# Performance work log

Measured on AMD Instinct MI355X. Metric: run time of the kernel, lower is better.

Reference implementation:

```python
import jax, jax.numpy as jnp
import numpy as np


def setup_inputs() -> dict:
    key = jax.random.key(0)
    k1, k2, k3 = jax.random.split(key, 3)
    B, H, S, D = 2, 8, 4096, 64
    queries = jax.random.normal(k1, (B, H, S, D), dtype=jnp.float32)
    keys = jax.random.normal(k2, (B, H, S, D), dtype=jnp.float32)
    values = jax.random.normal(k3, (B, H, S, D), dtype=jnp.float32)
    mask = jnp.zeros((1, 1, S, S), dtype=jnp.float32)
    return {"queries": queries, "keys": keys, "values": values, "d_k": D, "mask": mask}


def reference(queries, keys, values, d_k, mask):
    # scores: [B, H, Sq, Sk]
    scale = 1.0 / jnp.sqrt(jnp.asarray(d_k, dtype=queries.dtype))
    scores = jnp.einsum("bhqd,bhkd->bhqk", queries, keys) * scale
    scores = scores + (-1e9) * mask  # additive mask, broadcasts over B, H
    weights = jax.nn.softmax(scores, axis=-1)
    return jnp.einsum("bhqk,bhkd->bhqd", weights, values)
```

## Files before the change

kernel.cpp:

```cpp
#include <hip/hip_runtime.h>

#define S_LEN 4096
#define DHEAD 64
#define BK    64
#define NT    (S_LEN / BK)
#define NBH   16
#define KPAD  72
#define BQ    128
#define TILE_HALFS (BK * DHEAD)

typedef __fp16   pk16x2 __attribute__((ext_vector_type(2)));
typedef _Float16 half4v __attribute__((ext_vector_type(4)));
typedef _Float16 half8  __attribute__((ext_vector_type(8)));
typedef float    f32x4  __attribute__((ext_vector_type(4)));
typedef float    f32x16 __attribute__((ext_vector_type(16)));
typedef unsigned uint2v __attribute__((ext_vector_type(2)));

#define MFMA32(a, b, c) __builtin_amdgcn_mfma_f32_32x32x16_f16(a, b, c, 0, 0, 0)

__device__ __forceinline__ unsigned pk2u(float a, float b) {
    union { pk16x2 p; unsigned u; } x;
    x.p = __builtin_amdgcn_cvt_pkrtz(a, b);
    return x.u;
}

__device__ __forceinline__ uint2v pls(unsigned x, unsigned y) {
    return __builtin_amdgcn_permlane32_swap(x, y, false, false);
}
__device__ __forceinline__ float xmax32(float v) {
    uint2v r = pls(__float_as_uint(v), __float_as_uint(v));
    return fmaxf(__uint_as_float(r.x), __uint_as_float(r.y));
}
__device__ __forceinline__ float xadd32(float v) {
    uint2v r = pls(__float_as_uint(v), __float_as_uint(v));
    return __uint_as_float(r.x) + __uint_as_float(r.y);
}

__global__ void mask_flag_kernel(const float4* __restrict__ mask, int* __restrict__ flag) {
    const long stride = 2048L * 256;
    long i = (long)blockIdx.x * 256 + threadIdx.x;
    int nz = 0;
    #pragma unroll
    for (int it = 0; it < 8; ++it) {
        float4 a = mask[i + it * stride];
        nz |= (a.x != 0.f) | (a.y != 0.f) | (a.z != 0.f) | (a.w != 0.f);
    }
    if (__any(nz)) {
        if ((threadIdx.x & 63) == 0) atomicOr(flag, 1);
    }
}

__global__ __launch_bounds__(512, 2) void attn32f_kernel(
    const float* __restrict__ Q, const float* __restrict__ K,
    const float* __restrict__ V, const int* __restrict__ dkp,
    const float* __restrict__ mask, const int* __restrict__ maskflag,
    float* __restrict__ O)
{
    const int bid = blockIdx.x;
    const int L   = (bid & 7) * 64 + (bid >> 3);
    const int bh  = L >> 5;
    const int qt  = L & 31;

    const int tid  = threadIdx.x;
    const int hf   = tid >> 8;
    const int t    = tid & 255;
    const int w    = (tid >> 6) & 3;
    const int lane = tid & 63;
    const int l31  = lane & 31;
    const int h    = lane >> 5;
    const int cx   = lane & 7;
    const int vkey = (l31 ^ (l31 >> 3)) & 7;

    const int HT  = NT / 2;
    const int kt0 = hf * HT;

    const long gbase = (long)bh * S_LEN * DHEAD;
    const float* Qh = Q + gbase;
    const float* Kh = K + gbase;
    const float* Vh = V + gbase;

    const int q0 = qt * 128 + w * 32;
    const float csq  = rsqrtf((float)dkp[0]) * 1.44269504088896f;
    const float mfac = -1e9f * 1.44269504088896f;
    const bool use_mask = (maskflag[0] != 0);

    __shared__ __align__(16) _Float16 KT[2][2][TILE_HALFS];
    __shared__ __align__(16) _Float16 VT[2][2][TILE_HALFS];

    half8 qf[4];
    #pragma unroll
    for (int ks = 0; ks < 4; ++ks) {
        const float4* src = (const float4*)(Qh + (long)(q0 + l31) * DHEAD + ks * 16 + h * 8);
        float4 a = src[0], b = src[1];
        union { unsigned u[4]; half8 h8; } u;
        u.u[0] = pk2u(a.x * csq, a.y * csq);
        u.u[1] = pk2u(a.z * csq, a.w * csq);
        u.u[2] = pk2u(b.x * csq, b.y * csq);
        u.u[3] = pk2u(b.z * csq, b.w * csq);
        qf[ks] = u.h8;
    }

    const int kr  = t >> 2;
    const int ks4 = t & 3;
    const int vrp = t >> 3;
    const int vdq = t & 7;
    const float* Kb = Kh + (long)kr * DHEAD + ks4 * 16;
    const float* Vb = Vh + (long)(2 * vrp) * DHEAD + vdq * 8;
    const int kcol0 = (((2 * ks4)     ^ (kr & 7)) << 3);
    const int kcol1 = (((2 * ks4 + 1) ^ (kr & 7)) << 3);
    const int vd0   = vdq * 8;
    const int voct  = vrp >> 2;
    const int vlow  = (2 * vrp) & 7;

    float4 kf[4], vf[4];
    auto load_tile = [&](int kt) {
        const float4* kp  = (const float4*)(Kb + (long)kt * TILE_HALFS);
        kf[0] = kp[0]; kf[1] = kp[1]; kf[2] = kp[2]; kf[3] = kp[3];
        const float4* vp0 = (const float4*)(Vb + (long)kt * TILE_HALFS);
        const float4* vp1 = (const float4*)(Vb + (long)kt * TILE_HALFS + DHEAD);
        vf[0] = vp0[0]; vf[1] = vp0[1]; vf[2] = vp1[0]; vf[3] = vp1[1];
    };
    auto store_tile = [&](int bb) {
        union { unsigned u[4]; half8 h8; } u0, u1;
        u0.u[0] = pk2u(kf[0].x, kf[0].y);
        u0.u[1] = pk2u(kf[0].z, kf[0].w);
        u0.u[2] = pk2u(kf[1].x, kf[1].y);
        u0.u[3] = pk2u(kf[1].z, kf[1].w);
        u1.u[0] = pk2u(kf[2].x, kf[2].y);
        u1.u[1] = pk2u(kf[2].z, kf[2].w);
        u1.u[2] = pk2u(kf[3].x, kf[3].y);
        u1.u[3] = pk2u(kf[3].z, kf[3].w);
        *(half8*)&KT[hf][bb][kr * 64 + kcol0] = u0.h8;
        *(half8*)&KT[hf][bb][kr * 64 + kcol1] = u1.h8;
        _Float16* vt = &VT[hf][bb][0];
        #define VCOL(j) ((((voct ^ (j) ^ vdq) & 7) << 3) + vlow)
        *(pk16x2*)&vt[(vd0 + 0) * 64 + VCOL(0)] = __builtin_amdgcn_cvt_pkrtz(vf[0].x, vf[2].x);
        *(pk16x2*)&vt[(vd0 + 1) * 64 + VCOL(1)] = __builtin_amdgcn_cvt_pkrtz(vf[0].y, vf[2].y);
        *(pk16x2*)&vt[(vd0 + 2) * 64 + VCOL(2)] = __builtin_amdgcn_cvt_pkrtz(vf[0].z, vf[2].z);
        *(pk16x2*)&vt[(vd0 + 3) * 64 + VCOL(3)] = __builtin_amdgcn_cvt_pkrtz(vf[0].w, vf[2].w);
        *(pk16x2*)&vt[(vd0 + 4) * 64 + VCOL(4)] = __builtin_amdgcn_cvt_pkrtz(vf[1].x, vf[3].x);
        *(pk16x2*)&vt[(vd0 + 5) * 64 + VCOL(5)] = __builtin_amdgcn_cvt_pkrtz(vf[1].y, vf[3].y);
        *(pk16x2*)&vt[(vd0 + 6) * 64 + VCOL(6)] = __builtin_amdgcn_cvt_pkrtz(vf[1].z, vf[3].z);
        *(pk16x2*)&vt[(vd0 + 7) * 64 + VCOL(7)] = __builtin_amdgcn_cvt_pkrtz(vf[1].w, vf[3].w);
        #undef VCOL
    };

    f32x16 o0 = {0.f,0.f,0.f,0.f,0.f,0.f,0.f,0.f,0.f,0.f,0.f,0.f,0.f,0.f,0.f,0.f};
    f32x16 o1 = o0;
    float m_i = -INFINITY;
    float l_i = 0.0f;

    load_tile(kt0);
    store_tile(0);
    __syncthreads();

    for (int lt = 0; lt < HT; ++lt) {
        const int kt = kt0 + lt;
        const int b  = lt & 1;
        if (lt + 1 < HT) load_tile(kt + 1);

        f32x16 s0 = {0.f,0.f,0.f,0.f,0.f,0.f,0.f,0.f,0.f,0.f,0.f,0.f,0.f,0.f,0.f,0.f};
        f32x16 s1 = s0;
        __builtin_amdgcn_s_setprio(1);
        #pragma unroll
        for (int ks = 0; ks < 4; ++ks) {
            const int off = (((2 * ks + h) ^ cx) << 3);
            half8 a0 = *(const half8*)&KT[hf][b][(l31 << 6) + off];
            half8 a1 = *(const half8*)&KT[hf][b][2048 + (l31 << 6) + off];
            s0 = MFMA32(a0, qf[ks], s0);
            s1 = MFMA32(a1, qf[ks], s1);
        }
        __builtin_amdgcn_s_setprio(0);

        if (lt + 1 < HT) store_tile(b ^ 1);

        if (use_mask) {
            const float* mrow = mask + (long)(q0 + l31) * S_LEN + kt * BK;
            #pragma unroll
            for (int r = 0; r < 16; ++r) {
                const int k = (r & 3) + ((r >> 2) << 3) + (h << 2);
                s0[r] += mfac * mrow[k];
                s1[r] += mfac * mrow[32 + k];
            }
        }

        {
            float tt[8];
            #pragma unroll
            for (int i = 0; i < 8; ++i)
                tt[i] = fmaxf(fmaxf(s0[2*i], s0[2*i+1]), fmaxf(s1[2*i], s1[2*i+1]));
            float mx = fmaxf(fmaxf(fmaxf(tt[0], tt[1]), fmaxf(tt[2], tt[3])),
                             fmaxf(fmaxf(tt[4], tt[5]), fmaxf(tt[6], tt[7])));
            mx = xmax32(mx);
            const bool need = __any(mx > m_i + 8.0f);
            const float mnew = need ? fmaxf(m_i, mx) : m_i;
            float ra = 0.f, rb = 0.f;
            #pragma unroll
            for (int r = 0; r < 16; ++r) {
                float p0 = __builtin_amdgcn_exp2f(s0[r] - mnew);
                float p1 = __builtin_amdgcn_exp2f(s1[r] - mnew);
                s0[r] = p0; s1[r] = p1;
                ra += p0; rb += p1;
            }
            float rsum = xadd32(ra + rb);
            if (need) {
                const float alpha = __builtin_amdgcn_exp2f(m_i - mnew);
                #pragma unroll
                for (int r = 0; r < 16; ++r) {
                    const int qr = (r & 3) + ((r >> 2) << 3) + (h << 2);
                    float a_r = __shfl(alpha, qr, 64);
                    o0[r] *= a_r; o1[r] *= a_r;
                }
                l_i = alpha * l_i + rsum;
                m_i = mnew;
            } else {
                l_i += rsum;
            }
        }

        unsigned wp[16];
        #pragma unroll
        for (int d = 0; d < 8; ++d) {
            wp[d]     = pk2u(s0[2*d], s0[2*d+1]);
            wp[8 + d] = pk2u(s1[2*d], s1[2*d+1]);
        }

        __builtin_amdgcn_s_setprio(1);
        #pragma unroll
        for (int si = 0; si < 4; ++si) {
            const int bs = (si >> 1) * 8 + (si & 1) * 4;
            uint2v r0 = pls(wp[bs + 0], wp[bs + 2]);
            uint2v r1 = pls(wp[bs + 1], wp[bs + 3]);
            union { unsigned u[4]; half8 h8; } pa;
            pa.u[0] = r0.x; pa.u[1] = r1.x; pa.u[2] = r0.y; pa.u[3] = r1.y;
            const int voff = (((2 * si + h) ^ vkey) << 3);
            half8 v0 = *(const half8*)&VT[hf][b][(l31 << 6) + voff];
            half8 v1 = *(const half8*)&VT[hf][b][2048 + (l31 << 6) + (voff ^ 32)];
            o0 = MFMA32(pa.h8, v0, o0);
            o1 = MFMA32(pa.h8, v1, o1);
        }
        __builtin_amdgcn_s_setprio(0);

        if (lt + 1 < HT) __syncthreads();
    }

    float*  comb = (float*)&KT[0][0][0];
    float2* mlA  = (float2*)&VT[0][0][0];
    float2* mlB  = mlA + 128;

    __syncthreads();
    if (hf == 1) {
        #pragma unroll
        for (int r = 0; r < 16; ++r) {
            const int qr = (r & 3) + ((r >> 2) << 3) + (h << 2);
            comb[w * 2048 + qr * 64 + l31]      = o0[r];
            comb[w * 2048 + qr * 64 + 32 + l31] = o1[r];
        }
        if (h == 0) mlB[w * 32 + l31] = make_float2(m_i, l_i);
    } else {
        if (h == 0) mlA[w * 32 + l31] = make_float2(m_i, l_i);
    }
    __syncthreads();

    if (hf == 0) {
        float* dst = O + gbase;
        #pragma unroll
        for (int r = 0; r < 16; ++r) {
            const int qr = (r & 3) + ((r >> 2) << 3) + (h << 2);
            const float2 ml1 = mlA[w * 32 + qr];
            const float2 ml2 = mlB[w * 32 + qr];
            const float m   = fmaxf(ml1.x, ml2.x);
            const float a1  = __builtin_amdgcn_exp2f(ml1.x - m);
            const float a2  = __builtin_amdgcn_exp2f(ml2.x - m);
            const float inv = __builtin_amdgcn_rcpf(ml1.y * a1 + ml2.y * a2);
            const float p0  = comb[w * 2048 + qr * 64 + l31];
            const float p1  = comb[w * 2048 + qr * 64 + 32 + l31];
            const long row = (long)(q0 + qr) * DHEAD;
            dst[row + l31]      = (o0[r] * a1 + p0 * a2) * inv;
            dst[row + 32 + l31] = (o1[r] * a1 + p1 * a2) * inv;
        }
    }
}

__global__ __launch_bounds__(256, 2) void attn_kernel_fb(
    const float* __restrict__ Q, const float* __restrict__ K,
    const float* __restrict__ V, const int* __restrict__ dk,
    const float* __restrict__ mask, const int* __restrict__ maskflag,
    float* __restrict__ O)
{
    const int qt   = blockIdx.x;
    const int bh   = blockIdx.y;
    const int tid  = threadIdx.x;
    const int wave = tid >> 6;
    const int lane = tid & 63;
    const int l15  = lane & 15;
    const int quad = lane >> 4;

    const long base = (long)bh * S_LEN * DHEAD;
    const float* Qh = Q + base;
    const float* Kh = K + base;
    const float* Vh = V + base;
    float*       Oh = O + base;

    const int q0 = qt * BQ + wave * 32;
    const float csq  = rsqrtf((float)dk[0]) * 1.44269504088896f;
    const float mfac = -1e9f * 1.44269504088896f;
    const bool use_mask = (maskflag[0] != 0);

    __shared__ __align__(16) _Float16 Kt[2][BK][KPAD];
    __shared__ __align__(16) _Float16 Vt[2][DHEAD * KPAD];
    __shared__ __align__(16) _Float16 Pw[4][32][KPAD];

    half8 qf[2][2];
    #pragma unroll
    for (int f = 0; f < 2; ++f) {
        #pragma unroll
        for (int kc = 0; kc < 2; ++kc) {
            const float4* src = (const float4*)(Qh + (long)(q0 + f*16 + l15) * DHEAD + kc*32 + quad*8);
            float4 a = src[0], b = src[1];
            union { pk16x2 p[4]; half8 h; } u;
            u.p[0] = __builtin_amdgcn_cvt_pkrtz(a.x*csq, a.y*csq);
            u.p[1] = __builtin_amdgcn_cvt_pkrtz(a.z*csq, a.w*csq);
            u.p[2] = __builtin_amdgcn_cvt_pkrtz(b.x*csq, b.y*csq);
            u.p[3] = __builtin_amdgcn_cvt_pkrtz(b.z*csq, b.w*csq);
            qf[f][kc] = u.h;
        }
    }

    const int kr  = tid >> 2;
    const int ks  = tid & 3;
    const int vrp = tid >> 3;
    const int vdq = tid & 7;
    const float* Kb = Kh + (long)kr * DHEAD + ks * 16;
    const float* Vb = Vh + (long)(2 * vrp) * DHEAD + vdq * 8;
    const int vcol = (((vrp >> 2) ^ vdq) << 3) + ((2 * vrp) & 7);
    const int vd0  = vdq * 8;

    float4 kf[4], vf[4];
    auto load_tile = [&](int kt) {
        const float4* kp  = (const float4*)(Kb + (long)kt * BK * DHEAD);
        kf[0] = kp[0]; kf[1] = kp[1]; kf[2] = kp[2]; kf[3] = kp[3];
        const float4* vp0 = (const float4*)(Vb + (long)kt * BK * DHEAD);
        const float4* vp1 = (const float4*)(Vb + (long)kt * BK * DHEAD + DHEAD);
        vf[0] = vp0[0]; vf[1] = vp0[1]; vf[2] = vp1[0]; vf[3] = vp1[1];
    };
    auto store_tile = [&](int b) {
        union { pk16x2 p[4]; half8 h; } u0, u1;
        u0.p[0] = __builtin_amdgcn_cvt_pkrtz(kf[0].x, kf[0].y);
        u0.p[1] = __builtin_amdgcn_cvt_pkrtz(kf[0].z, kf[0].w);
        u0.p[2] = __builtin_amdgcn_cvt_pkrtz(kf[1].x, kf[1].y);
        u0.p[3] = __builtin_amdgcn_cvt_pkrtz(kf[1].z, kf[1].w);
        u1.p[0] = __builtin_amdgcn_cvt_pkrtz(kf[2].x, kf[2].y);
        u1.p[1] = __builtin_amdgcn_cvt_pkrtz(kf[2].z, kf[2].w);
        u1.p[2] = __builtin_amdgcn_cvt_pkrtz(kf[3].x, kf[3].y);
        u1.p[3] = __builtin_amdgcn_cvt_pkrtz(kf[3].z, kf[3].w);
        *(half8*)&Kt[b][kr][ks*16]     = u0.h;
        *(half8*)&Kt[b][kr][ks*16 + 8] = u1.h;
        _Float16* vt = &Vt[b][0];
        *(pk16x2*)&vt[(vd0+0)*KPAD + vcol] = __builtin_amdgcn_cvt_pkrtz(vf[0].x, vf[2].x);
        *(pk16x2*)&vt[(vd0+1)*KPAD + vcol] = __builtin_amdgcn_cvt_pkrtz(vf[0].y, vf[2].y);
        *(pk16x2*)&vt[(vd0+2)*KPAD + vcol] = __builtin_amdgcn_cvt_pkrtz(vf[0].z, vf[2].z);
        *(pk16x2*)&vt[(vd0+3)*KPAD + vcol] = __builtin_amdgcn_cvt_pkrtz(vf[0].w, vf[2].w);
        *(pk16x2*)&vt[(vd0+4)*KPAD + vcol] = __builtin_amdgcn_cvt_pkrtz(vf[1].x, vf[3].x);
        *(pk16x2*)&vt[(vd0+5)*KPAD + vcol] = __builtin_amdgcn_cvt_pkrtz(vf[1].y, vf[3].y);
        *(pk16x2*)&vt[(vd0+6)*KPAD + vcol] = __builtin_amdgcn_cvt_pkrtz(vf[1].z, vf[3].z);
        *(pk16x2*)&vt[(vd0+7)*KPAD + vcol] = __builtin_amdgcn_cvt_pkrtz(vf[1].w, vf[3].w);
    };

    f32x4 o[2][4];
    #pragma unroll
    for (int f = 0; f < 2; ++f)
        #pragma unroll
        for (int dt = 0; dt < 4; ++dt) o[f][dt] = (f32x4){0.f, 0.f, 0.f, 0.f};
    float m_i[2] = {-INFINITY, -INFINITY};
    float l_i[2] = {0.0f, 0.0f};

    load_tile(0);
    store_tile(0);
    __syncthreads();

    for (int kt = 0; kt < NT; ++kt) {
        const int b = kt & 1;
        if (kt + 1 < NT) load_tile(kt + 1);

        f32x4 st[2][4];
        #pragma unroll
        for (int f = 0; f < 2; ++f)
            #pragma unroll
            for (int nt = 0; nt < 4; ++nt) st[f][nt] = (f32x4){0.f,0.f,0.f,0.f};
        #pragma unroll
        for (int nt = 0; nt < 4; ++nt) {
            #pragma unroll
            for (int kc = 0; kc < 2; ++kc) {
                half8 af = *(const half8*)&Kt[b][nt*16 + l15][kc*32 + quad*8];
                st[0][nt] = __builtin_amdgcn_mfma_f32_16x16x32_f16(af, qf[0][kc], st[0][nt], 0, 0, 0);
                st[1][nt] = __builtin_amdgcn_mfma_f32_16x16x32_f16(af, qf[1][kc], st[1][nt], 0, 0, 0);
            }
        }

        if (use_mask) {
            #pragma unroll
            for (int f = 0; f < 2; ++f) {
                const long mrow = (long)(q0 + f*16 + l15) * S_LEN + kt*BK;
                #pragma unroll
                for (int nt = 0; nt < 4; ++nt)
                    #pragma unroll
                    for (int r = 0; r < 4; ++r)
                        st[f][nt][r] += mfac * mask[mrow + nt*16 + quad*4 + r];
            }
        }

        float alpha[2];
        #pragma unroll
        for (int f = 0; f < 2; ++f) {
            float mx = fmaxf(fmaxf(fmaxf(st[f][0][0], st[f][0][1]), fmaxf(st[f][0][2], st[f][0][3])),
                             fmaxf(fmaxf(st[f][1][0], st[f][1][1]), fmaxf(st[f][1][2], st[f][1][3])));
            float mx2 = fmaxf(fmaxf(fmaxf(st[f][2][0], st[f][2][1]), fmaxf(st[f][2][2], st[f][2][3])),
                              fmaxf(fmaxf(st[f][3][0], st[f][3][1]), fmaxf(st[f][3][2], st[f][3][3])));
            mx = fmaxf(mx, mx2);
            mx = fmaxf(mx, __shfl_xor(mx, 16, 64));
            mx = fmaxf(mx, __shfl_xor(mx, 32, 64));
            float mnew = fmaxf(m_i[f], mx);
            float rsum = 0.0f;
            #pragma unroll
            for (int nt = 0; nt < 4; ++nt) {
                #pragma unroll
                for (int r = 0; r < 4; ++r) {
                    float p = __builtin_amdgcn_exp2f(st[f][nt][r] - mnew);
                    st[f][nt][r] = p;
                    rsum += p;
                }
            }
            rsum += __shfl_xor(rsum, 16, 64);
            rsum += __shfl_xor(rsum, 32, 64);
            alpha[f] = __builtin_amdgcn_exp2f(m_i[f] - mnew);
            l_i[f] = alpha[f] * l_i[f] + rsum;
            m_i[f] = mnew;
        }

        #pragma unroll
        for (int f = 0; f < 2; ++f)
            #pragma unroll
            for (int r = 0; r < 4; ++r) {
                float a_r = __shfl(alpha[f], quad*4 + r, 64);
                #pragma unroll
                for (int dt = 0; dt < 4; ++dt) o[f][dt][r] *= a_r;
            }

        #pragma unroll
        for (int f = 0; f < 2; ++f)
            #pragma unroll
            for (int nt = 0; nt < 4; ++nt) {
                union { pk16x2 p[2]; half4v h; } up;
                up.p[0] = __builtin_amdgcn_cvt_pkrtz(st[f][nt][0], st[f][nt][1]);
                up.p[1] = __builtin_amdgcn_cvt_pkrtz(st[f][nt][2], st[f][nt][3]);
                *(half4v*)&Pw[wave][f*16 + l15][nt*16 + quad*4] = up.h;
            }

        #pragma unroll
        for (int kc2 = 0; kc2 < 2; ++kc2) {
            half8 pa0 = *(const half8*)&Pw[wave][l15][kc2*32 + quad*8];
            half8 pa1 = *(const half8*)&Pw[wave][16 + l15][kc2*32 + quad*8];
            #pragma unroll
            for (int dt = 0; dt < 4; ++dt) {
                const int row = dt*16 + l15;
                const int pb  = (4*kc2 + quad) ^ (row >> 3);
                half8 vb = *(const half8*)&Vt[b][row*KPAD + pb*8];
                o[0][dt] = __builtin_amdgcn_mfma_f32_16x16x32_f16(pa0, vb, o[0][dt], 0, 0, 0);
                o[1][dt] = __builtin_amdgcn_mfma_f32_16x16x32_f16(pa1, vb, o[1][dt], 0, 0, 0);
            }
        }

        if (kt + 1 < NT) {
            store_tile((kt + 1) & 1);
            __syncthreads();
        }
    }

    #pragma unroll
    for (int f = 0; f < 2; ++f) {
        #pragma unroll
        for (int r = 0; r < 4; ++r) {
            float lq = __shfl(l_i[f], quad*4 + r, 64);
            float linv = __builtin_amdgcn_rcpf(lq);
            const long row = (long)(q0 + f*16 + quad*4 + r) * DHEAD;
            #pragma unroll
            for (int dt = 0; dt < 4; ++dt)
                Oh[row + dt*16 + l15] = o[f][dt][r] * linv;
        }
    }
}

extern "C" void kernel_launch(void* const* d_in, const int* in_sizes, int n_in,
                              void* d_out, int out_size, void* d_ws, size_t ws_size,
                              hipStream_t stream) {
    const float* Q    = (const float*)d_in[0];
    const float* K    = (const float*)d_in[1];
    const float* V    = (const float*)d_in[2];
    const int*   dk   = (const int*)d_in[3];
    const float* mask = (const float*)d_in[4];
    float* out = (float*)d_out;
    int* flag = (int*)d_ws;

    (void)hipMemsetAsync(flag, 0, sizeof(int), stream);
    mask_flag_kernel<<<2048, 256, 0, stream>>>((const float4*)mask, flag);

    if (ws_size >= 256) {
        attn32f_kernel<<<512, 512, 0, stream>>>(Q, K, V, dk, mask, flag, out);
    } else {
        dim3 grid(S_LEN / BQ, NBH);
        attn_kernel_fb<<<grid, 256, 0, stream>>>(Q, K, V, dk, mask, flag, out);
    }
}
```

Measured before the change: 281.3 us.

## Drop split-K two-half workgroups; run single 256-thread block over all key tiles

```diff
diff --git a/kernel.cpp b/kernel.cpp
--- a/kernel.cpp
+++ b/kernel.cpp
@@ -4,15 +4,10 @@
 #define DHEAD 64
 #define BK    64
 #define NT    (S_LEN / BK)
-#define NBH   16
-#define KPAD  72
-#define BQ    128
 #define TILE_HALFS (BK * DHEAD)
 
 typedef __fp16   pk16x2 __attribute__((ext_vector_type(2)));
-typedef _Float16 half4v __attribute__((ext_vector_type(4)));
 typedef _Float16 half8  __attribute__((ext_vector_type(8)));
-typedef float    f32x4  __attribute__((ext_vector_type(4)));
 typedef float    f32x16 __attribute__((ext_vector_type(16)));
 typedef unsigned uint2v __attribute__((ext_vector_type(2)));
 
@@ -50,7 +45,7 @@
     }
 }
 
-__global__ __launch_bounds__(512, 2) void attn32f_kernel(
+__global__ __launch_bounds__(256, 2) void attn32s_kernel(
     const float* __restrict__ Q, const float* __restrict__ K,
     const float* __restrict__ V, const int* __restrict__ dkp,
     const float* __restrict__ mask, const int* __restrict__ maskflag,
@@ -62,18 +57,13 @@
     const int qt  = L & 31;
 
     const int tid  = threadIdx.x;
-    const int hf   = tid >> 8;
-    const int t    = tid & 255;
-    const int w    = (tid >> 6) & 3;
+    const int w    = tid >> 6;
     const int lane = tid & 63;
     const int l31  = lane & 31;
     const int h    = lane >> 5;
     const int cx   = lane & 7;
     const int vkey = (l31 ^ (l31 >> 3)) & 7;
 
-    const int HT  = NT / 2;
-    const int kt0 = hf * HT;
-
     const long gbase = (long)bh * S_LEN * DHEAD;
     const float* Qh = Q + gbase;
     const float* Kh = K + gbase;
@@ -84,8 +74,8 @@
     const float mfac = -1e9f * 1.44269504088896f;
     const bool use_mask = (maskflag[0] != 0);
 
-    __shared__ __align__(16) _Float16 KT[2][2][TILE_HALFS];
-    __shared__ __align__(16) _Float16 VT[2][2][TILE_HALFS];
+    __shared__ __align__(16) _Float16 KT[2][TILE_HALFS];
+    __shared__ __align__(16) _Float16 VT[2][TILE_HALFS];
 
     half8 qf[4];
     #pragma unroll
@@ -100,10 +90,10 @@
         qf[ks] = u.h8;
     }
 
-    const int kr  = t >> 2;
-    const int ks4 = t & 3;
-    const int vrp = t >> 3;
-    const int vdq = t & 7;
+    const int kr  = tid >> 2;
+    const int ks4 = tid & 3;
+    const int vrp = tid >> 3;
+    const int vdq = tid & 7;
     const float* Kb = Kh + (long)kr * DHEAD + ks4 * 16;
     const float* Vb = Vh + (long)(2 * vrp) * DHEAD + vdq * 8;
     const int kcol0 = (((2 * ks4)     ^ (kr & 7)) << 3);
@@ -130,9 +120,9 @@
         u1.u[1] = pk2u(kf[2].z, kf[2].w);
         u1.u[2] = pk2u(kf[3].x, kf[3].y);
         u1.u[3] = pk2u(kf[3].z, kf[3].w);
-        *(half8*)&KT[hf][bb][kr * 64 + kcol0] = u0.h8;
-        *(half8*)&KT[hf][bb][kr * 64 + kcol1] = u1.h8;
-        _Float16* vt = &VT[hf][bb][0];
+        *(half8*)&KT[bb][kr * 64 + kcol0] = u0.h8;
+        *(half8*)&KT[bb][kr * 64 + kcol1] = u1.h8;
+        _Float16* vt = &VT[bb][0];
         #define VCOL(j) ((((voct ^ (j) ^ vdq) & 7) << 3) + vlow)
         *(pk16x2*)&vt[(vd0 + 0) * 64 + VCOL(0)] = __builtin_amdgcn_cvt_pkrtz(vf[0].x, vf[2].x);
         *(pk16x2*)&vt[(vd0 + 1) * 64 + VCOL(1)] = __builtin_amdgcn_cvt_pkrtz(vf[0].y, vf[2].y);
@@ -150,14 +140,13 @@
     float m_i = -INFINITY;
     float l_i = 0.0f;
 
-    load_tile(kt0);
+    load_tile(0);
     store_tile(0);
     __syncthreads();
 
-    for (int lt = 0; lt < HT; ++lt) {
-        const int kt = kt0 + lt;
-        const int b  = lt & 1;
-        if (lt + 1 < HT) load_tile(kt + 1);
+    for (int kt = 0; kt < NT; ++kt) {
+        const int b = kt & 1;
+        if (kt + 1 < NT) load_tile(kt + 1);
 
         f32x16 s0 = {0.f,0.f,0.f,0.f,0.f,0.f,0.f,0.f,0.f,0.f,0.f,0.f,0.f,0.f,0.f,0.f};
         f32x16 s1 = s0;
@@ -165,14 +154,14 @@
         #pragma unroll
         for (int ks = 0; ks < 4; ++ks) {
             const int off = (((2 * ks + h) ^ cx) << 3);
-            half8 a0 = *(const half8*)&KT[hf][b][(l31 << 6) + off];
-            half8 a1 = *(const half8*)&KT[hf][b][2048 + (l31 << 6) + off];
+            half8 a0 = *(const half8*)&KT[b][(l31 << 6) + off];
+            half8 a1 = *(const half8*)&KT[b][2048 + (l31 << 6) + off];
             s0 = MFMA32(a0, qf[ks], s0);
             s1 = MFMA32(a1, qf[ks], s1);
         }
         __builtin_amdgcn_s_setprio(0);
 
-        if (lt + 1 < HT) store_tile(b ^ 1);
+        if (kt + 1 < NT) store_tile(b ^ 1);
 
         if (use_mask) {
             const float* mrow = mask + (long)(q0 + l31) * S_LEN + kt * BK;
@@ -234,260 +223,25 @@
             union { unsigned u[4]; half8 h8; } pa;
             pa.u[0] = r0.x; pa.u[1] = r1.x; pa.u[2] = r0.y; pa.u[3] = r1.y;
             const int voff = (((2 * si + h) ^ vkey) << 3);
-            half8 v0 = *(const half8*)&VT[hf][b][(l31 << 6) + voff];
-            half8 v1 = *(const half8*)&VT[hf][b][2048 + (l31 << 6) + (voff ^ 32)];
+            half8 v0 = *(const half8*)&VT[b][(l31 << 6) + voff];
+            half8 v1 = *(const half8*)&VT[b][2048 + (l31 << 6) + (voff ^ 32)];
             o0 = MFMA32(pa.h8, v0, o0);
             o1 = MFMA32(pa.h8, v1, o1);
         }
         __builtin_amdgcn_s_setprio(0);
 
-        if (lt + 1 < HT) __syncthreads();
-    }
-
-    float*  comb = (float*)&KT[0][0][0];
-    float2* mlA  = (float2*)&VT[0][0][0];
-    float2* mlB  = mlA + 128;
-
-    __syncthreads();
-    if (hf == 1) {
-        #pragma unroll
-        for (int r = 0; r < 16; ++r) {
-            const int qr = (r & 3) + ((r >> 2) << 3) + (h << 2);
-            comb[w * 2048 + qr * 64 + l31]      = o0[r];
-            comb[w * 2048 + qr * 64 + 32 + l31] = o1[r];
-        }
-        if (h == 0) mlB[w * 32 + l31] = make_float2(m_i, l_i);
-    } else {
-        if (h == 0) mlA[w * 32 + l31] = make_float2(m_i, l_i);
-    }
-    __syncthreads();
-
-    if (hf == 0) {
-        float* dst = O + gbase;
-        #pragma unroll
-        for (int r = 0; r < 16; ++r) {
-            const int qr = (r & 3) + ((r >> 2) << 3) + (h << 2);
-            const float2 ml1 = mlA[w * 32 + qr];
-            const float2 ml2 = mlB[w * 32 + qr];
-            const float m   = fmaxf(ml1.x, ml2.x);
-            const float a1  = __builtin_amdgcn_exp2f(ml1.x - m);
-            const float a2  = __builtin_amdgcn_exp2f(ml2.x - m);
-            const float inv = __builtin_amdgcn_rcpf(ml1.y * a1 + ml2.y * a2);
-            const float p0  = comb[w * 2048 + qr * 64 + l31];
-            const float p1  = comb[w * 2048 + qr * 64 + 32 + l31];
-            const long row = (long)(q0 + qr) * DHEAD;
-            dst[row + l31]      = (o0[r] * a1 + p0 * a2) * inv;
-            dst[row + 32 + l31] = (o1[r] * a1 + p1 * a2) * inv;
-        }
-    }
-}
-
-__global__ __launch_bounds__(256, 2) void attn_kernel_fb(
-    const float* __restrict__ Q, const float* __restrict__ K,
-    const float* __restrict__ V, const int* __restrict__ dk,
-    const float* __restrict__ mask, const int* __restrict__ maskflag,
-    float* __restrict__ O)
-{
-    const int qt   = blockIdx.x;
-    const int bh   = blockIdx.y;
-    const int tid  = threadIdx.x;
-    const int wave = tid >> 6;
-    const int lane = tid & 63;
-    const int l15  = lane & 15;
-    const int quad = lane >> 4;
-
-    const long base = (long)bh * S_LEN * DHEAD;
-    const float* Qh = Q + base;
-    const float* Kh = K + base;
-    const float* Vh = V + base;
-    float*       Oh = O + base;
-
-    const int q0 = qt * BQ + wave * 32;
-    const float csq  = rsqrtf((float)dk[0]) * 1.44269504088896f;
-    const float mfac = -1e9f * 1.44269504088896f;
-    const bool use_mask = (maskflag[0] != 0);
-
-    __shared__ __align__(16) _Float16 Kt[2][BK][KPAD];
-    __shared__ __align__(16) _Float16 Vt[2][DHEAD * KPAD];
-    __shared__ __align__(16) _Float16 Pw[4][32][KPAD];
-
-    half8 qf[2][2];
+        if (kt + 1 < NT) __syncthreads();
+    }
+
+    float* dst = O + gbase;
     #pragma unroll
-    for (int f = 0; f < 2; ++f) {
-        #pragma unroll
-        for (int kc = 0; kc < 2; ++kc) {
-            const float4* src = (const float4*)(Qh + (long)(q0 + f*16 + l15) * DHEAD + kc*32 + quad*8);
-            float4 a = src[0], b = src[1];
-            union { pk16x2 p[4]; half8 h; } u;
-            u.p[0] = __builtin_amdgcn_cvt_pkrtz(a.x*csq, a.y*csq);
-            u.p[1] = __builtin_amdgcn_cvt_pkrtz(a.z*csq, a.w*csq);
-            u.p[2] = __builtin_amdgcn_cvt_pkrtz(b.x*csq, b.y*csq);
-            u.p[3] = __builtin_amdgcn_cvt_pkrtz(b.z*csq, b.w*csq);
-            qf[f][kc] = u.h;
-        }
-    }
-
-    const int kr  = tid >> 2;
-    const int ks  = tid & 3;
-    const int vrp = tid >> 3;
-    const int vdq = tid & 7;
-    const float* Kb = Kh + (long)kr * DHEAD + ks * 16;
-    const float* Vb = Vh + (long)(2 * vrp) * DHEAD + vdq * 8;
-    const int vcol = (((vrp >> 2) ^ vdq) << 3) + ((2 * vrp) & 7);
-    const int vd0  = vdq * 8;
-
-    float4 kf[4], vf[4];
-    auto load_tile = [&](int kt) {
-        const float4* kp  = (const float4*)(Kb + (long)kt * BK * DHEAD);
-        kf[0] = kp[0]; kf[1] = kp[1]; kf[2] = kp[2]; kf[3] = kp[3];
-        const float4* vp0 = (const float4*)(Vb + (long)kt * BK * DHEAD);
-        const float4* vp1 = (const float4*)(Vb + (long)kt * BK * DHEAD + DHEAD);
-        vf[0] = vp0[0]; vf[1] = vp0[1]; vf[2] = vp1[0]; vf[3] = vp1[1];
-    };
-    auto store_tile = [&](int b) {
-        union { pk16x2 p[4]; half8 h; } u0, u1;
-        u0.p[0] = __builtin_amdgcn_cvt_pkrtz(kf[0].x, kf[0].y);
-        u0.p[1] = __builtin_amdgcn_cvt_pkrtz(kf[0].z, kf[0].w);
-        u0.p[2] = __builtin_amdgcn_cvt_pkrtz(kf[1].x, kf[1].y);
-        u0.p[3] = __builtin_amdgcn_cvt_pkrtz(kf[1].z, kf[1].w);
-        u1.p[0] = __builtin_amdgcn_cvt_pkrtz(kf[2].x, kf[2].y);
-        u1.p[1] = __builtin_amdgcn_cvt_pkrtz(kf[2].z, kf[2].w);
-        u1.p[2] = __builtin_amdgcn_cvt_pkrtz(kf[3].x, kf[3].y);
-        u1.p[3] = __builtin_amdgcn_cvt_pkrtz(kf[3].z, kf[3].w);
-        *(half8*)&Kt[b][kr][ks*16]     = u0.h;
-        *(half8*)&Kt[b][kr][ks*16 + 8] = u1.h;
-        _Float16* vt = &Vt[b][0];
-        *(pk16x2*)&vt[(vd0+0)*KPAD + vcol] = __builtin_amdgcn_cvt_pkrtz(vf[0].x, vf[2].x);
-        *(pk16x2*)&vt[(vd0+1)*KPAD + vcol] = __builtin_amdgcn_cvt_pkrtz(vf[0].y, vf[2].y);
-        *(pk16x2*)&vt[(vd0+2)*KPAD + vcol] = __builtin_amdgcn_cvt_pkrtz(vf[0].z, vf[2].z);
-        *(pk16x2*)&vt[(vd0+3)*KPAD + vcol] = __builtin_amdgcn_cvt_pkrtz(vf[0].w, vf[2].w);
-        *(pk16x2*)&vt[(vd0+4)*KPAD + vcol] = __builtin_amdgcn_cvt_pkrtz(vf[1].x, vf[3].x);
-        *(pk16x2*)&vt[(vd0+5)*KPAD + vcol] = __builtin_amdgcn_cvt_pkrtz(vf[1].y, vf[3].y);
-        *(pk16x2*)&vt[(vd0+6)*KPAD + vcol] = __builtin_amdgcn_cvt_pkrtz(vf[1].z, vf[3].z);
-        *(pk16x2*)&vt[(vd0+7)*KPAD + vcol] = __builtin_amdgcn_cvt_pkrtz(vf[1].w, vf[3].w);
-    };
-
-    f32x4 o[2][4];
-    #pragma unroll
-    for (int f = 0; f < 2; ++f)
-        #pragma unroll
-        for (int dt = 0; dt < 4; ++dt) o[f][dt] = (f32x4){0.f, 0.f, 0.f, 0.f};
-    float m_i[2] = {-INFINITY, -INFINITY};
-    float l_i[2] = {0.0f, 0.0f};
-
-    load_tile(0);
-    store_tile(0);
-    __syncthreads();
-
-    for (int kt = 0; kt < NT; ++kt) {
-        const int b = kt & 1;
-        if (kt + 1 < NT) load_tile(kt + 1);
-
-        f32x4 st[2][4];
-        #pragma unroll
-        for (int f = 0; f < 2; ++f)
-            #pragma unroll
-            for (int nt = 0; nt < 4; ++nt) st[f][nt] = (f32x4){0.f,0.f,0.f,0.f};
-        #pragma unroll
-        for (int nt = 0; nt < 4; ++nt) {
-            #pragma unroll
-            for (int kc = 0; kc < 2; ++kc) {
-                half8 af = *(const half8*)&Kt[b][nt*16 + l15][kc*32 + quad*8];
-                st[0][nt] = __builtin_amdgcn_mfma_f32_16x16x32_f16(af, qf[0][kc], st[0][nt], 0, 0, 0);
-                st[1][nt] = __builtin_amdgcn_mfma_f32_16x16x32_f16(af, qf[1][kc], st[1][nt], 0, 0, 0);
-            }
-        }
-
-        if (use_mask) {
-            #pragma unroll
-            for (int f = 0; f < 2; ++f) {
-                const long mrow = (long)(q0 + f*16 + l15) * S_LEN + kt*BK;
-                #pragma unroll
-                for (int nt = 0; nt < 4; ++nt)
-                    #pragma unroll
-                    for (int r = 0; r < 4; ++r)
-                        st[f][nt][r] += mfac * mask[mrow + nt*16 + quad*4 + r];
-            }
-        }
-
-        float alpha[2];
-        #pragma unroll
-        for (int f = 0; f < 2; ++f) {
-            float mx = fmaxf(fmaxf(fmaxf(st[f][0][0], st[f][0][1]), fmaxf(st[f][0][2], st[f][0][3])),
-                             fmaxf(fmaxf(st[f][1][0], st[f][1][1]), fmaxf(st[f][1][2], st[f][1][3])));
-            float mx2 = fmaxf(fmaxf(fmaxf(st[f][2][0], st[f][2][1]), fmaxf(st[f][2][2], st[f][2][3])),
-                              fmaxf(fmaxf(st[f][3][0], st[f][3][1]), fmaxf(st[f][3][2], st[f][3][3])));
-            mx = fmaxf(mx, mx2);
-            mx = fmaxf(mx, __shfl_xor(mx, 16, 64));
-            mx = fmaxf(mx, __shfl_xor(mx, 32, 64));
-            float mnew = fmaxf(m_i[f], mx);
-            float rsum = 0.0f;
-            #pragma unroll
-            for (int nt = 0; nt < 4; ++nt) {
-                #pragma unroll
-                for (int r = 0; r < 4; ++r) {
-                    float p = __builtin_amdgcn_exp2f(st[f][nt][r] - mnew);
-                    st[f][nt][r] = p;
-                    rsum += p;
-                }
-            }
-            rsum += __shfl_xor(rsum, 16, 64);
-            rsum += __shfl_xor(rsum, 32, 64);
-            alpha[f] = __builtin_amdgcn_exp2f(m_i[f] - mnew);
-            l_i[f] = alpha[f] * l_i[f] + rsum;
-            m_i[f] = mnew;
-        }
-
-        #pragma unroll
-        for (int f = 0; f < 2; ++f)
-            #pragma unroll
-            for (int r = 0; r < 4; ++r) {
-                float a_r = __shfl(alpha[f], quad*4 + r, 64);
-                #pragma unroll
-                for (int dt = 0; dt < 4; ++dt) o[f][dt][r] *= a_r;
-            }
-
-        #pragma unroll
-        for (int f = 0; f < 2; ++f)
-            #pragma unroll
-            for (int nt = 0; nt < 4; ++nt) {
-                union { pk16x2 p[2]; half4v h; } up;
-                up.p[0] = __builtin_amdgcn_cvt_pkrtz(st[f][nt][0], st[f][nt][1]);
-                up.p[1] = __builtin_amdgcn_cvt_pkrtz(st[f][nt][2], st[f][nt][3]);
-                *(half4v*)&Pw[wave][f*16 + l15][nt*16 + quad*4] = up.h;
-            }
-
-        #pragma unroll
-        for (int kc2 = 0; kc2 < 2; ++kc2) {
-            half8 pa0 = *(const half8*)&Pw[wave][l15][kc2*32 + quad*8];
-            half8 pa1 = *(const half8*)&Pw[wave][16 + l15][kc2*32 + quad*8];
-            #pragma unroll
-            for (int dt = 0; dt < 4; ++dt) {
-                const int row = dt*16 + l15;
-                const int pb  = (4*kc2 + quad) ^ (row >> 3);
-                half8 vb = *(const half8*)&Vt[b][row*KPAD + pb*8];
-                o[0][dt] = __builtin_amdgcn_mfma_f32_16x16x32_f16(pa0, vb, o[0][dt], 0, 0, 0);
-                o[1][dt] = __builtin_amdgcn_mfma_f32_16x16x32_f16(pa1, vb, o[1][dt], 0, 0, 0);
-            }
-        }
-
-        if (kt + 1 < NT) {
-            store_tile((kt + 1) & 1);
-            __syncthreads();
-        }
-    }
-
-    #pragma unroll
-    for (int f = 0; f < 2; ++f) {
-        #pragma unroll
-        for (int r = 0; r < 4; ++r) {
-            float lq = __shfl(l_i[f], quad*4 + r, 64);
-            float linv = __builtin_amdgcn_rcpf(lq);
-            const long row = (long)(q0 + f*16 + quad*4 + r) * DHEAD;
-            #pragma unroll
-            for (int dt = 0; dt < 4; ++dt)
-                Oh[row + dt*16 + l15] = o[f][dt][r] * linv;
-        }
+    for (int r = 0; r < 16; ++r) {
+        const int qr = (r & 3) + ((r >> 2) << 3) + (h << 2);
+        float lq = __shfl(l_i, qr, 64);
+        float inv = __builtin_amdgcn_rcpf(lq);
+        const long row = (long)(q0 + qr) * DHEAD;
+        dst[row + l31]      = o0[r] * inv;
+        dst[row + 32 + l31] = o1[r] * inv;
     }
 }
 
@@ -505,10 +259,5 @@
     (void)hipMemsetAsync(flag, 0, sizeof(int), stream);
     mask_flag_kernel<<<2048, 256, 0, stream>>>((const float4*)mask, flag);
 
-    if (ws_size >= 256) {
-        attn32f_kernel<<<512, 512, 0, stream>>>(Q, K, V, dk, mask, flag, out);
-    } else {
-        dim3 grid(S_LEN / BQ, NBH);
-        attn_kernel_fb<<<grid, 256, 0, stream>>>(Q, K, V, dk, mask, flag, out);
-    }
-}
+    attn32s_kernel<<<512, 256, 0, stream>>>(Q, K, V, dk, mask, flag, out);
+}
```

Measured after the change: 239.4 us, median of 2. -14.9%, faster.
